# Kernel tuning notes

Measured on AMD Instinct MI355X. Metric: run time of the kernel, lower is better.

The kernel has to match this reference:

```python
import jax, jax.numpy as jnp
import numpy as np

EMBED_DIM = 1024
NUM_HEADS = 16
HEAD_DIM = EMBED_DIM // NUM_HEADS
MLP_HIDDEN = 4096


def layer_norm(x, gamma, beta, eps=1e-5):
    mu = jnp.mean(x, axis=-1, keepdims=True)
    var = jnp.var(x, axis=-1, keepdims=True)
    return (x - mu) / jnp.sqrt(var + eps) * gamma + beta


def setup_inputs() -> dict:
    key = jax.random.key(0)
    ks = jax.random.split(key, 16)
    d, h = EMBED_DIM, MLP_HIDDEN
    s = 0.02
    inp = {
        "x": jax.random.normal(ks[0], (2, 2048, d), dtype=jnp.float32),
        "ln1_g": jnp.ones((d,), jnp.float32),
        "ln1_b": jnp.zeros((d,), jnp.float32),
        "ln2_g": jnp.ones((d,), jnp.float32),
        "ln2_b": jnp.zeros((d,), jnp.float32),
        "Wq": jax.random.normal(ks[1], (d, d), jnp.float32) * s,
        "bq": jnp.zeros((d,), jnp.float32),
        "Wk": jax.random.normal(ks[2], (d, d), jnp.float32) * s,
        "bk": jnp.zeros((d,), jnp.float32),
        "Wv": jax.random.normal(ks[3], (d, d), jnp.float32) * s,
        "bv": jnp.zeros((d,), jnp.float32),
        "Wo": jax.random.normal(ks[4], (d, d), jnp.float32) * s,
        "bo": jnp.zeros((d,), jnp.float32),
        "W1": jax.random.normal(ks[5], (d, h), jnp.float32) * s,
        "b1": jnp.zeros((h,), jnp.float32),
        "W2": jax.random.normal(ks[6], (h, d), jnp.float32) * s,
        "b2": jnp.zeros((d,), jnp.float32),
    }
    return inp


def reference(x, ln1_g, ln1_b, ln2_g, ln2_b, Wq, bq, Wk, bk, Wv, bv, Wo, bo, W1, b1, W2, b2):
    B, T, C = x.shape
    H, Dh = NUM_HEADS, HEAD_DIM
    # attention branch
    xn = layer_norm(x, ln1_g, ln1_b)
    q = (xn @ Wq + bq).reshape(B, T, H, Dh).transpose(0, 2, 1, 3)  # [B,H,T,Dh]
    k = (xn @ Wk + bk).reshape(B, T, H, Dh).transpose(0, 2, 1, 3)
    v = (xn @ Wv + bv).reshape(B, T, H, Dh).transpose(0, 2, 1, 3)
    scores = jnp.einsum('bhtd,bhsd->bhts', q, k) / jnp.sqrt(jnp.float32(Dh))
    attn = jax.nn.softmax(scores, axis=-1)
    out = jnp.einsum('bhts,bhsd->bhtd', attn, v)
    out = out.transpose(0, 2, 1, 3).reshape(B, T, C)
    x = x + out @ Wo + bo
    # MLP branch
    xn2 = layer_norm(x, ln2_g, ln2_b)
    x = x + jax.nn.relu(xn2 @ W1 + b1) @ W2 + b2
    return x
```

## Files before the change

kernel.cpp:

```cpp
#include <hip/hip_runtime.h>

typedef float f32x4 __attribute__((ext_vector_type(4)));
typedef __bf16 bf16x8 __attribute__((ext_vector_type(8)));

constexpr int TT   = 2048;
constexpr int CC   = 1024;
constexpr int HIDN = 4096;
constexpr int MM   = 4096;
constexpr int NQKV = 3072;

union U84 { uint32_t u[4]; bf16x8 v; };

__device__ inline uint32_t cvt_pk_bf16(float lo, float hi) {
  uint32_t r;
  asm("v_cvt_pk_bf16_f32 %0, %1, %2" : "=v"(r) : "v"(lo), "v"(hi));
  return r;
}
__device__ inline ushort f2bf(float f) { return (ushort)(cvt_pk_bf16(f, 0.f) & 0xffffu); }
__device__ inline float bfbits2f(uint32_t bits) {
  union { uint32_t u; float f; } c; c.u = bits; return c.f;
}
__device__ inline float exp2_fast(float x) {
  float r;
  asm("v_exp_f32 %0, %1" : "=v"(r) : "v"(x));
  return r;
}

#define AS1C(p) ((__attribute__((address_space(1))) void*)(p))
#define AS3(p)  ((__attribute__((address_space(3))) void*)(p))

__global__ __launch_bounds__(256) void prep_weights(const float* __restrict__ Wq,
                                                    const float* __restrict__ Wk,
                                                    const float* __restrict__ Wv,
                                                    const float* __restrict__ Wo,
                                                    const float* __restrict__ W1,
                                                    const float* __restrict__ W2,
                                                    const float* __restrict__ bq,
                                                    const float* __restrict__ bk,
                                                    const float* __restrict__ bv,
                                                    const float* __restrict__ x,
                                                    const float* __restrict__ g1,
                                                    const float* __restrict__ b1v,
                                                    ushort* __restrict__ WqkvT,
                                                    ushort* __restrict__ WoT,
                                                    ushort* __restrict__ W1T,
                                                    ushort* __restrict__ W2T,
                                                    float* __restrict__ Bqkv,
                                                    ushort* __restrict__ Xn) {
  const int id = blockIdx.x;
  const int t = threadIdx.x;
  if (id >= 12300) {
    const int row = id - 12300;
    float4 v = reinterpret_cast<const float4*>(x + (size_t)row * CC)[t];
    float s  = v.x + v.y + v.z + v.w;
    float ss = v.x * v.x + v.y * v.y + v.z * v.z + v.w * v.w;
#pragma unroll
    for (int off = 32; off; off >>= 1) {
      s  += __shfl_down(s, off);
      ss += __shfl_down(ss, off);
    }
    __shared__ float red[16];
    const int wid = t >> 6, lane = t & 63;
    if (lane == 0) { red[wid] = s; red[8 + wid] = ss; }
    __syncthreads();
    if (t == 0) {
      red[0] = red[0] + red[1] + red[2] + red[3];
      red[8] = red[8] + red[9] + red[10] + red[11];
    }
    __syncthreads();
    const float mu   = red[0] * (1.0f / CC);
    const float var  = red[8] * (1.0f / CC) - mu * mu;
    const float rstd = rsqrtf(var + 1e-5f);
    float4 gg = reinterpret_cast<const float4*>(g1)[t];
    float4 bb = reinterpret_cast<const float4*>(b1v)[t];
    uint2 st;
    st.x = cvt_pk_bf16((v.x - mu) * rstd * gg.x + bb.x, (v.y - mu) * rstd * gg.y + bb.y);
    st.y = cvt_pk_bf16((v.z - mu) * rstd * gg.z + bb.z, (v.w - mu) * rstd * gg.w + bb.w);
    *reinterpret_cast<uint2*>(Xn + (size_t)row * CC + t * 4) = st;
    return;
  }
  if (id >= 12288) {
    const int i = (id - 12288) * 256 + t;
    Bqkv[i] = (i < 1024) ? bq[i] : ((i < 2048) ? bk[i - 1024] : bv[i - 2048]);
    return;
  }
  const float* W; ushort* out; int Kd, Nd, bx, by, rowOff = 0;
  if (id < 4096) {
    const int which = id >> 10, sub = id & 1023;
    bx = sub & 31; by = sub >> 5; Kd = 1024; Nd = 1024;
    if (which == 0)      { W = Wq; out = WqkvT; rowOff = 0; }
    else if (which == 1) { W = Wk; out = WqkvT; rowOff = 1024; }
    else if (which == 2) { W = Wv; out = WqkvT; rowOff = 2048; }
    else                 { W = Wo; out = WoT; }
  } else if (id < 8192) {
    const int sub = id - 4096; bx = sub & 127; by = sub >> 7;
    W = W1; out = W1T; Kd = 1024; Nd = 4096;
  } else {
    const int sub = id - 8192; bx = sub & 31; by = sub >> 5;
    W = W2; out = W2T; Kd = 4096; Nd = 1024;
  }
  const int n0 = bx * 32, k0 = by * 32;
  __shared__ float Ts[32][33];
  {
    const int r = t >> 3, cb = (t & 7) * 4;
    float4 v = *reinterpret_cast<const float4*>(W + (size_t)(k0 + r) * Nd + n0 + cb);
    Ts[r][cb + 0] = v.x; Ts[r][cb + 1] = v.y; Ts[r][cb + 2] = v.z; Ts[r][cb + 3] = v.w;
  }
  __syncthreads();
  {
    const int nl = t >> 3, kb = (t & 7) * 4;
    uint2 st;
    st.x = cvt_pk_bf16(Ts[kb + 0][nl], Ts[kb + 1][nl]);
    st.y = cvt_pk_bf16(Ts[kb + 2][nl], Ts[kb + 3][nl]);
    *reinterpret_cast<uint2*>(out + (size_t)(rowOff + n0 + nl) * Kd + k0 + kb) = st;
  }
}

template <int BN, bool RELU, bool VOUT, bool PARTIAL>
__global__ __launch_bounds__(512, 2) void gemm_8w(const ushort* __restrict__ A,
                                                  const ushort* __restrict__ Bt,
                                                  const float* __restrict__ bias,
                                                  ushort* __restrict__ outp,
                                                  ushort* __restrict__ Vt,
                                                  ushort* __restrict__ P1,
                                                  ushort* __restrict__ P2,
                                                  ushort* __restrict__ P3,
                                                  int N, int K, int Kchunk) {
  constexpr int WCOLS = BN / 4;
  constexpr int NF    = WCOLS / 16;
  constexpr int BCH   = BN / 64;
  constexpr int BUFB  = 32768 + BN * 128;
  __shared__ char lds[2 * BUFB];
  const int t = threadIdx.x, lane = t & 63, w = t >> 6;
  const int g = lane >> 4, i16 = lane & 15;
  const int wr = w >> 2, wc = w & 3;
  const int nwg  = gridDim.x * gridDim.y;
  const int orig = blockIdx.y * gridDim.x + blockIdx.x;
  const int sw   = (orig & 7) * (nwg >> 3) + (orig >> 3);
  const int row0 = (sw / gridDim.x) * 256, col0 = (sw % gridDim.x) * BN;
  const int kstart = PARTIAL ? blockIdx.z * Kchunk : 0;
  const int NT = (PARTIAL ? Kchunk : K) >> 6;
  ushort* __restrict__ Out = outp;
  if (PARTIAL) Out = (blockIdx.z == 0) ? outp : (blockIdx.z == 1) ? P1
              : (blockIdx.z == 2) ? P2 : P3;

  const ushort* aG[4];
  const ushort* bG[BCH];
#pragma unroll
  for (int i = 0; i < 4; ++i) {
    const int c = t + 512 * i;
    const int r = c >> 3, ssw = (c & 7) ^ (r & 7);
    aG[i] = A + (size_t)(row0 + r) * K + kstart + ssw * 8;
  }
#pragma unroll
  for (int i = 0; i < BCH; ++i) {
    const int c = t + 512 * i;
    const int r = c >> 3, ssw = (c & 7) ^ (r & 7);
    bG[i] = Bt + (size_t)(col0 + r) * K + kstart + ssw * 8;
  }

  int aoff[8][2], boff[NF][2];
#pragma unroll
  for (int mf = 0; mf < 8; ++mf) {
    const int R = wr * 128 + mf * 16 + i16;
#pragma unroll
    for (int kk = 0; kk < 2; ++kk)
      aoff[mf][kk] = R * 128 + (((kk << 2) | g) ^ (R & 7)) * 16;
  }
#pragma unroll
  for (int nf = 0; nf < NF; ++nf) {
    const int Cn = wc * WCOLS + nf * 16 + i16;
#pragma unroll
    for (int kk = 0; kk < 2; ++kk)
      boff[nf][kk] = Cn * 128 + (((kk << 2) | g) ^ (Cn & 7)) * 16;
  }

  f32x4 acc[8][NF] = {};

  auto STAGE = [&](int bi, int kt) {
    char* aB = lds + bi * BUFB;
    char* bB = aB + 32768;
    const int ko = kt * 64;
#pragma unroll
    for (int i = 0; i < 4; ++i)
      __builtin_amdgcn_global_load_lds(AS1C(aG[i] + ko), AS3(aB + i * 8192 + w * 1024), 16, 0, 0);
#pragma unroll
    for (int i = 0; i < BCH; ++i)
      __builtin_amdgcn_global_load_lds(AS1C(bG[i] + ko), AS3(bB + i * 8192 + w * 1024), 16, 0, 0);
  };

  STAGE(0, 0);

  for (int kt = 0; kt < NT; ++kt) {
    const int cur = kt & 1;
    if (kt + 1 < NT) {
      STAGE(cur ^ 1, kt + 1);
      if constexpr (BN == 256) asm volatile("s_waitcnt vmcnt(8)" ::: "memory");
      else                     asm volatile("s_waitcnt vmcnt(7)" ::: "memory");
    } else {
      asm volatile("s_waitcnt vmcnt(0)" ::: "memory");
    }
    asm volatile("s_barrier" ::: "memory");
    __builtin_amdgcn_sched_barrier(0);

    const char* aB = (const char*)lds + cur * BUFB;
    const char* bB = aB + 32768;
    bf16x8 b4[NF][2], a4[4][2];
#pragma unroll
    for (int nf = 0; nf < NF; ++nf)
#pragma unroll
      for (int kk = 0; kk < 2; ++kk)
        b4[nf][kk] = *reinterpret_cast<const bf16x8*>(bB + boff[nf][kk]);
#pragma unroll
    for (int mf = 0; mf < 4; ++mf)
#pragma unroll
      for (int kk = 0; kk < 2; ++kk)
        a4[mf][kk] = *reinterpret_cast<const bf16x8*>(aB + aoff[mf][kk]);
    __builtin_amdgcn_s_setprio(1);
#pragma unroll
    for (int mf = 0; mf < 4; ++mf)
#pragma unroll
      for (int nf = 0; nf < NF; ++nf)
#pragma unroll
        for (int kk = 0; kk < 2; ++kk)
          acc[mf][nf] = __builtin_amdgcn_mfma_f32_16x16x32_bf16(a4[mf][kk], b4[nf][kk], acc[mf][nf], 0, 0, 0);
    __builtin_amdgcn_s_setprio(0);
    asm volatile("s_barrier" ::: "memory");
    __builtin_amdgcn_sched_barrier(0);
#pragma unroll
    for (int mf = 0; mf < 4; ++mf)
#pragma unroll
      for (int kk = 0; kk < 2; ++kk)
        a4[mf][kk] = *reinterpret_cast<const bf16x8*>(aB + aoff[mf + 4][kk]);
    __builtin_amdgcn_s_setprio(1);
#pragma unroll
    for (int mf = 0; mf < 4; ++mf)
#pragma unroll
      for (int nf = 0; nf < NF; ++nf)
#pragma unroll
        for (int kk = 0; kk < 2; ++kk)
          acc[mf + 4][nf] = __builtin_amdgcn_mfma_f32_16x16x32_bf16(a4[mf][kk], b4[nf][kk], acc[mf + 4][nf], 0, 0, 0);
    __builtin_amdgcn_s_setprio(0);
    asm volatile("s_barrier" ::: "memory");
    __builtin_amdgcn_sched_barrier(0);
  }

  const int qcol0 = col0 + wc * WCOLS;

  if constexpr (VOUT) {
#pragma unroll
    for (int nf = 0; nf < NF; ++nf) {
      const int ncol = qcol0 + nf * 16 + i16;
      const float bb = bias[ncol];
      if (ncol >= 2048) {
        const int d = ncol - 2048;
        const int hh = d >> 6, dd = d & 63;
#pragma unroll
        for (int mf = 0; mf < 8; ++mf) {
          const int mrow = row0 + wr * 128 + mf * 16 + 4 * g;
          const int bb_ = mrow >> 11, tok = mrow & 2047;
          uint2 st;
          st.x = cvt_pk_bf16(acc[mf][nf][0] + bb, acc[mf][nf][1] + bb);
          st.y = cvt_pk_bf16(acc[mf][nf][2] + bb, acc[mf][nf][3] + bb);
          *reinterpret_cast<uint2*>(Vt + (size_t)((bb_ * 16 + hh) * 64 + dd) * TT + tok) = st;
        }
      } else {
#pragma unroll
        for (int mf = 0; mf < 8; ++mf) {
          const int mrow = row0 + wr * 128 + mf * 16 + 4 * g;
#pragma unroll
          for (int r = 0; r < 4; ++r)
            Out[(size_t)(mrow + r) * N + ncol] = f2bf(acc[mf][nf][r] + bb);
        }
      }
    }
    return;
  } else {
    float* Lf = (float*)(lds + w * 4096);
    const int rr2 = lane >> 2, q = lane & 3;
#pragma unroll
    for (int mf = 0; mf < 8; ++mf) {
#pragma unroll
      for (int nf = 0; nf < NF; ++nf)
#pragma unroll
        for (int r = 0; r < 4; ++r) {
          const int row = 4 * g + r;
          Lf[row * 64 + ((16 * nf + i16) ^ ((row & 7) << 2))] = acc[mf][nf][r];
        }
      asm volatile("s_waitcnt lgkmcnt(0)" ::: "memory");
      uint32_t u[8];
#pragma unroll
      for (int j = 0; j < 4; ++j) {
        f32x4 v = *reinterpret_cast<const f32x4*>(Lf + rr2 * 64 + ((q * 16 + 4 * j) ^ ((rr2 & 7) << 2)));
        float e0 = v[0], e1 = v[1], e2 = v[2], e3 = v[3];
        if (!PARTIAL) {
          const float4 b4v = *reinterpret_cast<const float4*>(bias + qcol0 + q * 16 + 4 * j);
          e0 += b4v.x; e1 += b4v.y; e2 += b4v.z; e3 += b4v.w;
          if (RELU) {
            e0 = fmaxf(e0, 0.f); e1 = fmaxf(e1, 0.f);
            e2 = fmaxf(e2, 0.f); e3 = fmaxf(e3, 0.f);
          }
        }
        u[2 * j + 0] = cvt_pk_bf16(e0, e1);
        u[2 * j + 1] = cvt_pk_bf16(e2, e3);
      }
      const int mrow = row0 + wr * 128 + mf * 16 + rr2;
      ushort* orow = Out + (size_t)mrow * N + qcol0 + q * 16;
      uint4 s0; s0.x = u[0]; s0.y = u[1]; s0.z = u[2]; s0.w = u[3];
      uint4 s1; s1.x = u[4]; s1.y = u[5]; s1.z = u[6]; s1.w = u[7];
      *reinterpret_cast<uint4*>(orow) = s0;
      *reinterpret_cast<uint4*>(orow + 8) = s1;
      asm volatile("s_waitcnt lgkmcnt(0)" ::: "memory");
    }
  }
}

__device__ inline float bfsum4(uint32_t a, uint32_t b, uint32_t c, uint32_t d, bool hi) {
  if (hi) return bfbits2f(a & 0xffff0000u) + bfbits2f(b & 0xffff0000u) +
                 bfbits2f(c & 0xffff0000u) + bfbits2f(d & 0xffff0000u);
  return bfbits2f(a << 16) + bfbits2f(b << 16) + bfbits2f(c << 16) + bfbits2f(d << 16);
}

__global__ __launch_bounds__(256) void reduce_wo_ln(const ushort* __restrict__ P0,
                                                    const ushort* __restrict__ P1,
                                                    const ushort* __restrict__ P2,
                                                    const ushort* __restrict__ P3,
                                                    const float* __restrict__ x,
                                                    const float* __restrict__ bo,
                                                    const float* __restrict__ g,
                                                    const float* __restrict__ b,
                                                    float* __restrict__ X1f,
                                                    ushort* __restrict__ Xn) {
  const int row = blockIdx.x, t = threadIdx.x;
  const size_t off = (size_t)row * CC + t * 4;
  float4 v  = *reinterpret_cast<const float4*>(x + off);
  const uint2 q0 = *reinterpret_cast<const uint2*>(P0 + off);
  const uint2 q1 = *reinterpret_cast<const uint2*>(P1 + off);
  const uint2 q2 = *reinterpret_cast<const uint2*>(P2 + off);
  const uint2 q3 = *reinterpret_cast<const uint2*>(P3 + off);
  float4 bb = reinterpret_cast<const float4*>(bo)[t];
  v.x += bfsum4(q0.x, q1.x, q2.x, q3.x, false) + bb.x;
  v.y += bfsum4(q0.x, q1.x, q2.x, q3.x, true)  + bb.y;
  v.z += bfsum4(q0.y, q1.y, q2.y, q3.y, false) + bb.z;
  v.w += bfsum4(q0.y, q1.y, q2.y, q3.y, true)  + bb.w;
  *reinterpret_cast<float4*>(X1f + off) = v;

  float s  = v.x + v.y + v.z + v.w;
  float ss = v.x * v.x + v.y * v.y + v.z * v.z + v.w * v.w;
#pragma unroll
  for (int o = 32; o; o >>= 1) {
    s  += __shfl_down(s, o);
    ss += __shfl_down(ss, o);
  }
  __shared__ float red[16];
  const int wid = t >> 6, lane = t & 63;
  if (lane == 0) { red[wid] = s; red[8 + wid] = ss; }
  __syncthreads();
  if (t == 0) {
    red[0] = red[0] + red[1] + red[2] + red[3];
    red[8] = red[8] + red[9] + red[10] + red[11];
  }
  __syncthreads();
  const float mu   = red[0] * (1.0f / CC);
  const float var  = red[8] * (1.0f / CC) - mu * mu;
  const float rstd = rsqrtf(var + 1e-5f);
  float4 gg = reinterpret_cast<const float4*>(g)[t];
  float4 lb = reinterpret_cast<const float4*>(b)[t];
  uint2 st;
  st.x = cvt_pk_bf16((v.x - mu) * rstd * gg.x + lb.x, (v.y - mu) * rstd * gg.y + lb.y);
  st.y = cvt_pk_bf16((v.z - mu) * rstd * gg.z + lb.z, (v.w - mu) * rstd * gg.w + lb.w);
  *reinterpret_cast<uint2*>(Xn + off) = st;
}

__global__ __launch_bounds__(256) void reduce_fc2(const ushort* __restrict__ P0,
                                                  const ushort* __restrict__ P1,
                                                  const ushort* __restrict__ P2,
                                                  const ushort* __restrict__ P3,
                                                  const float* __restrict__ X1,
                                                  const float* __restrict__ b2,
                                                  float* __restrict__ out) {
  const int row = blockIdx.x, t = threadIdx.x;
  const size_t off = (size_t)row * CC + t * 4;
  float4 v  = *reinterpret_cast<const float4*>(X1 + off);
  const uint2 q0 = *reinterpret_cast<const uint2*>(P0 + off);
  const uint2 q1 = *reinterpret_cast<const uint2*>(P1 + off);
  const uint2 q2 = *reinterpret_cast<const uint2*>(P2 + off);
  const uint2 q3 = *reinterpret_cast<const uint2*>(P3 + off);
  float4 bb = reinterpret_cast<const float4*>(b2)[t];
  v.x += bfsum4(q0.x, q1.x, q2.x, q3.x, false) + bb.x;
  v.y += bfsum4(q0.x, q1.x, q2.x, q3.x, true)  + bb.y;
  v.z += bfsum4(q0.y, q1.y, q2.y, q3.y, false) + bb.z;
  v.w += bfsum4(q0.y, q1.y, q2.y, q3.y, true)  + bb.w;
  *reinterpret_cast<float4*>(out + off) = v;
}

__global__ __launch_bounds__(512, 4) void attn_full(const ushort* __restrict__ qkv,
                                                    const ushort* __restrict__ Vt,
                                                    ushort* __restrict__ attnb) {
  __shared__ ushort Ks[2][4096];
  __shared__ ushort Vs[2][4096];
  __shared__ uint32_t Ps[8][16][36];
  const int t = threadIdx.x, lane = t & 63, w = t >> 6;
  const int g = lane >> 4, iq = lane & 15;
  const int flat = blockIdx.x;
  const int work = (flat & 7) * 64 + (flat >> 3);
  const int bh = work >> 4;
  const int qt = work & 15;
  const int b = bh >> 4, h = bh & 15;

  bf16x8 qfrag[2];
  {
    const ushort* qrow = qkv + (size_t)(b * TT + qt * 128 + w * 16 + iq) * NQKV + h * 64;
    const float qs = 0.125f * 1.44269504f;
#pragma unroll
    for (int kk = 0; kk < 2; ++kk) {
      uint4 raw = *reinterpret_cast<const uint4*>(qrow + kk * 32 + g * 8);
      uint32_t rr[4] = {raw.x, raw.y, raw.z, raw.w};
      U84 tmp;
#pragma unroll
      for (int c = 0; c < 4; ++c) {
        float lo = bfbits2f(rr[c] << 16) * qs;
        float hi = bfbits2f(rr[c] & 0xffff0000u) * qs;
        tmp.u[c] = cvt_pk_bf16(lo, hi);
      }
      qfrag[kk] = tmp.v;
    }
  }

  const int sr1 = t >> 3, sc1 = t & 7;
  const int csw = (sc1 ^ (sr1 & 7)) * 8;
  const ushort* kbase = qkv + 1024 + h * 64;
  const ushort* vbase = Vt + (size_t)(bh * 64) * TT;

  auto STAGE = [&](int bi, int kt) {
    const size_t tok = (size_t)(b * TT + kt * 64);
    __builtin_amdgcn_global_load_lds(AS1C(kbase + (tok + sr1) * NQKV + csw),
                                     AS3((char*)&Ks[bi][0] + w * 1024), 16, 0, 0);
    __builtin_amdgcn_global_load_lds(AS1C(vbase + (size_t)sr1 * TT + kt * 64 + csw),
                                     AS3((char*)&Vs[bi][0] + w * 1024), 16, 0, 0);
  };

  uint32_t (*pw)[36] = Ps[w];
  const int wsw = (iq & 8) << 1;
  const int xsb = wsw << 2;
  const char* prow = (const char*)&pw[iq][0];

  float lrun = 0.f;
  f32x4 ot[4] = {};

  constexpr int NKT = TT / 64;
  STAGE(0, 0);

  for (int kt = 0; kt < NKT; ++kt) {
    const int cur = kt & 1;
    if (kt + 1 < NKT) {
      STAGE(cur ^ 1, kt + 1);
      asm volatile("s_waitcnt vmcnt(2)" ::: "memory");
    } else {
      asm volatile("s_waitcnt vmcnt(0)" ::: "memory");
    }
    asm volatile("s_barrier" ::: "memory");
    __builtin_amdgcn_sched_barrier(0);
    const char* Kc = (const char*)&Ks[cur][0];
    const char* Vc = (const char*)&Vs[cur][0];

    f32x4 sfr[4] = {};
    __builtin_amdgcn_s_setprio(1);
#pragma unroll
    for (int kk = 0; kk < 2; ++kk)
#pragma unroll
      for (int jf = 0; jf < 4; ++jf) {
        const int row = iq + 16 * jf;
        const int off = row * 128 + ((kk * 64 + g * 16) ^ ((row & 7) << 4));
        bf16x8 a = *reinterpret_cast<const bf16x8*>(Kc + off);
        sfr[jf] = __builtin_amdgcn_mfma_f32_16x16x32_bf16(a, qfrag[kk], sfr[jf], 0, 0, 0);
      }
    __builtin_amdgcn_s_setprio(0);

#pragma unroll
    for (int f = 0; f < 4; ++f) {
      float p0 = exp2_fast(sfr[f][0]);
      float p1 = exp2_fast(sfr[f][1]);
      float p2 = exp2_fast(sfr[f][2]);
      float p3 = exp2_fast(sfr[f][3]);
      lrun += (p0 + p1) + (p2 + p3);
      uint2 st2;
      st2.x = cvt_pk_bf16(p0, p1);
      st2.y = cvt_pk_bf16(p2, p3);
      *reinterpret_cast<uint2*>(&pw[iq][(8 * f + 2 * g) ^ wsw]) = st2;
    }
    asm volatile("s_waitcnt lgkmcnt(0)" ::: "memory");

    __builtin_amdgcn_s_setprio(1);
#pragma unroll
    for (int kk = 0; kk < 2; ++kk) {
      bf16x8 pb = *reinterpret_cast<const bf16x8*>(prow + ((kk * 64 + g * 16) ^ xsb));
#pragma unroll
      for (int df = 0; df < 4; ++df) {
        const int row = iq + 16 * df;
        const int off = row * 128 + ((kk * 64 + g * 16) ^ ((row & 7) << 4));
        bf16x8 a = *reinterpret_cast<const bf16x8*>(Vc + off);
        ot[df] = __builtin_amdgcn_mfma_f32_16x16x32_bf16(a, pb, ot[df], 0, 0, 0);
      }
    }
    __builtin_amdgcn_s_setprio(0);

    asm volatile("s_barrier" ::: "memory");
    __builtin_amdgcn_sched_barrier(0);
  }

  lrun += __shfl_xor(lrun, 16, 64);
  lrun += __shfl_xor(lrun, 32, 64);
  const int grow = b * TT + qt * 128 + w * 16 + iq;
  const float inv = 1.f / lrun;
  ushort* orow = attnb + (size_t)grow * CC + h * 64;
#pragma unroll
  for (int df = 0; df < 4; ++df) {
    uint2 st;
    st.x = cvt_pk_bf16(ot[df][0] * inv, ot[df][1] * inv);
    st.y = cvt_pk_bf16(ot[df][2] * inv, ot[df][3] * inv);
    *reinterpret_cast<uint2*>(orow + df * 16 + g * 4) = st;
  }
}

extern "C" void kernel_launch(void* const* d_in, const int* in_sizes, int n_in,
                              void* d_out, int out_size, void* d_ws, size_t ws_size,
                              hipStream_t stream) {
  const float* x     = (const float*)d_in[0];
  const float* ln1_g = (const float*)d_in[1];
  const float* ln1_b = (const float*)d_in[2];
  const float* ln2_g = (const float*)d_in[3];
  const float* ln2_b = (const float*)d_in[4];
  const float* Wq = (const float*)d_in[5];
  const float* bq = (const float*)d_in[6];
  const float* Wk = (const float*)d_in[7];
  const float* bk = (const float*)d_in[8];
  const float* Wv = (const float*)d_in[9];
  const float* bv = (const float*)d_in[10];
  const float* Wo = (const float*)d_in[11];
  const float* bo = (const float*)d_in[12];
  const float* W1 = (const float*)d_in[13];
  const float* b1 = (const float*)d_in[14];
  const float* W2 = (const float*)d_in[15];
  const float* b2 = (const float*)d_in[16];
  float* out = (float*)d_out;
  char* ws = (char*)d_ws;

  ushort* WqkvT = (ushort*)(ws + 0);
  ushort* WoT   = (ushort*)(ws + 6291456);
  ushort* W1T   = (ushort*)(ws + 8388608);
  ushort* W2T   = (ushort*)(ws + 16777216);
  float*  Bqkv  = (float*) (ws + 25165824);
  ushort* Xn    = (ushort*)(ws + 25178112);
  ushort* Attn  = (ushort*)(ws + 33566720);
  float*  X1f   = (float*) (ws + 41955328);
  ushort* Qkv   = (ushort*)(ws + 58732544);
  ushort* Vtb   = (ushort*)(ws + 83898368);
  ushort* Hid   = (ushort*)(ws + 58732544);
  ushort* WoP0  = (ushort*)(ws + 58732544);
  ushort* WoP1  = (ushort*)(ws + 67121152);
  ushort* WoP2  = (ushort*)(ws + 75509760);
  ushort* WoP3  = (ushort*)(ws + 83898368);
  ushort* F2P0  = (ushort*)(ws + 0);
  ushort* F2P1  = (ushort*)(ws + 8388608);
  ushort* F2P2  = (ushort*)(ws + 25178112);
  ushort* F2P3  = (ushort*)(ws + 33566720);

  const dim3 blk(256);

  prep_weights<<<dim3(16396), blk, 0, stream>>>(Wq, Wk, Wv, Wo, W1, W2, bq, bk, bv,
                                                x, ln1_g, ln1_b,
                                                WqkvT, WoT, W1T, W2T, Bqkv, Xn);
  gemm_8w<192, false, true, false><<<dim3(16, 16), dim3(512), 0, stream>>>(
      Xn, WqkvT, Bqkv, Qkv, Vtb, nullptr, nullptr, nullptr, NQKV, 1024, 0);
  attn_full<<<dim3(512), dim3(512), 0, stream>>>(Qkv, Vtb, Attn);
  gemm_8w<256, false, false, true><<<dim3(4, 16, 4), dim3(512), 0, stream>>>(
      Attn, WoT, nullptr, WoP0, nullptr, WoP1, WoP2, WoP3, 1024, 1024, 256);
  reduce_wo_ln<<<dim3(MM), blk, 0, stream>>>(WoP0, WoP1, WoP2, WoP3, x, bo, ln2_g, ln2_b, X1f, Xn);
  gemm_8w<256, true, false, false><<<dim3(16, 16), dim3(512), 0, stream>>>(
      Xn, W1T, b1, Hid, nullptr, nullptr, nullptr, nullptr, HIDN, 1024, 0);
  gemm_8w<256, false, false, true><<<dim3(4, 16, 4), dim3(512), 0, stream>>>(
      Hid, W2T, nullptr, F2P0, nullptr, F2P1, F2P2, F2P3, 1024, 4096, 1024);
  reduce_fc2<<<dim3(MM), blk, 0, stream>>>(F2P0, F2P1, F2P2, F2P3, X1f, b2, out);
}
```

Baseline: 222.6 us.

## Use BN=128 tiles with 2-way split-K for Wo and FC2 GEMMs

```diff
diff --git a/kernel.cpp b/kernel.cpp
--- a/kernel.cpp
+++ b/kernel.cpp
@@ -123,8 +123,6 @@
                                                   ushort* __restrict__ outp,
                                                   ushort* __restrict__ Vt,
                                                   ushort* __restrict__ P1,
-                                                  ushort* __restrict__ P2,
-                                                  ushort* __restrict__ P3,
                                                   int N, int K, int Kchunk) {
   constexpr int WCOLS = BN / 4;
   constexpr int NF    = WCOLS / 16;
@@ -140,9 +138,7 @@
   const int row0 = (sw / gridDim.x) * 256, col0 = (sw % gridDim.x) * BN;
   const int kstart = PARTIAL ? blockIdx.z * Kchunk : 0;
   const int NT = (PARTIAL ? Kchunk : K) >> 6;
-  ushort* __restrict__ Out = outp;
-  if (PARTIAL) Out = (blockIdx.z == 0) ? outp : (blockIdx.z == 1) ? P1
-              : (blockIdx.z == 2) ? P2 : P3;
+  ushort* __restrict__ Out = (PARTIAL && blockIdx.z) ? P1 : outp;
 
   const ushort* aG[4];
   const ushort* bG[BCH];
@@ -195,8 +191,9 @@
     const int cur = kt & 1;
     if (kt + 1 < NT) {
       STAGE(cur ^ 1, kt + 1);
-      if constexpr (BN == 256) asm volatile("s_waitcnt vmcnt(8)" ::: "memory");
-      else                     asm volatile("s_waitcnt vmcnt(7)" ::: "memory");
+      if constexpr (BN == 256)      asm volatile("s_waitcnt vmcnt(8)" ::: "memory");
+      else if constexpr (BN == 192) asm volatile("s_waitcnt vmcnt(7)" ::: "memory");
+      else                          asm volatile("s_waitcnt vmcnt(6)" ::: "memory");
     } else {
       asm volatile("s_waitcnt vmcnt(0)" ::: "memory");
     }
@@ -272,6 +269,19 @@
           for (int r = 0; r < 4; ++r)
             Out[(size_t)(mrow + r) * N + ncol] = f2bf(acc[mf][nf][r] + bb);
         }
+      }
+    }
+    return;
+  } else if constexpr (BN == 128) {
+#pragma unroll
+    for (int nf = 0; nf < NF; ++nf) {
+      const int ncol = qcol0 + nf * 16 + i16;
+#pragma unroll
+      for (int mf = 0; mf < 8; ++mf) {
+        const int mrow = row0 + wr * 128 + mf * 16 + 4 * g;
+#pragma unroll
+        for (int r = 0; r < 4; ++r)
+          Out[(size_t)(mrow + r) * N + ncol] = f2bf(acc[mf][nf][r]);
       }
     }
     return;
@@ -315,16 +325,13 @@
   }
 }
 
-__device__ inline float bfsum4(uint32_t a, uint32_t b, uint32_t c, uint32_t d, bool hi) {
-  if (hi) return bfbits2f(a & 0xffff0000u) + bfbits2f(b & 0xffff0000u) +
-                 bfbits2f(c & 0xffff0000u) + bfbits2f(d & 0xffff0000u);
-  return bfbits2f(a << 16) + bfbits2f(b << 16) + bfbits2f(c << 16) + bfbits2f(d << 16);
+__device__ inline float bfsum2(uint32_t a, uint32_t b, bool hi) {
+  if (hi) return bfbits2f(a & 0xffff0000u) + bfbits2f(b & 0xffff0000u);
+  return bfbits2f(a << 16) + bfbits2f(b << 16);
 }
 
 __global__ __launch_bounds__(256) void reduce_wo_ln(const ushort* __restrict__ P0,
                                                     const ushort* __restrict__ P1,
-                                                    const ushort* __restrict__ P2,
-                                                    const ushort* __restrict__ P3,
                                                     const float* __restrict__ x,
                                                     const float* __restrict__ bo,
                                                     const float* __restrict__ g,
@@ -336,13 +343,11 @@
   float4 v  = *reinterpret_cast<const float4*>(x + off);
   const uint2 q0 = *reinterpret_cast<const uint2*>(P0 + off);
   const uint2 q1 = *reinterpret_cast<const uint2*>(P1 + off);
-  const uint2 q2 = *reinterpret_cast<const uint2*>(P2 + off);
-  const uint2 q3 = *reinterpret_cast<const uint2*>(P3 + off);
   float4 bb = reinterpret_cast<const float4*>(bo)[t];
-  v.x += bfsum4(q0.x, q1.x, q2.x, q3.x, false) + bb.x;
-  v.y += bfsum4(q0.x, q1.x, q2.x, q3.x, true)  + bb.y;
-  v.z += bfsum4(q0.y, q1.y, q2.y, q3.y, false) + bb.z;
-  v.w += bfsum4(q0.y, q1.y, q2.y, q3.y, true)  + bb.w;
+  v.x += bfsum2(q0.x, q1.x, false) + bb.x;
+  v.y += bfsum2(q0.x, q1.x, true)  + bb.y;
+  v.z += bfsum2(q0.y, q1.y, false) + bb.z;
+  v.w += bfsum2(q0.y, q1.y, true)  + bb.w;
   *reinterpret_cast<float4*>(X1f + off) = v;
 
   float s  = v.x + v.y + v.z + v.w;
@@ -374,8 +379,6 @@
 
 __global__ __launch_bounds__(256) void reduce_fc2(const ushort* __restrict__ P0,
                                                   const ushort* __restrict__ P1,
-                                                  const ushort* __restrict__ P2,
-                                                  const ushort* __restrict__ P3,
                                                   const float* __restrict__ X1,
                                                   const float* __restrict__ b2,
                                                   float* __restrict__ out) {
@@ -384,13 +387,11 @@
   float4 v  = *reinterpret_cast<const float4*>(X1 + off);
   const uint2 q0 = *reinterpret_cast<const uint2*>(P0 + off);
   const uint2 q1 = *reinterpret_cast<const uint2*>(P1 + off);
-  const uint2 q2 = *reinterpret_cast<const uint2*>(P2 + off);
-  const uint2 q3 = *reinterpret_cast<const uint2*>(P3 + off);
   float4 bb = reinterpret_cast<const float4*>(b2)[t];
-  v.x += bfsum4(q0.x, q1.x, q2.x, q3.x, false) + bb.x;
-  v.y += bfsum4(q0.x, q1.x, q2.x, q3.x, true)  + bb.y;
-  v.z += bfsum4(q0.y, q1.y, q2.y, q3.y, false) + bb.z;
-  v.w += bfsum4(q0.y, q1.y, q2.y, q3.y, true)  + bb.w;
+  v.x += bfsum2(q0.x, q1.x, false) + bb.x;
+  v.y += bfsum2(q0.x, q1.x, true)  + bb.y;
+  v.z += bfsum2(q0.y, q1.y, false) + bb.z;
+  v.w += bfsum2(q0.y, q1.y, true)  + bb.w;
   *reinterpret_cast<float4*>(out + off) = v;
 }
 
@@ -559,12 +560,8 @@
   ushort* Hid   = (ushort*)(ws + 58732544);
   ushort* WoP0  = (ushort*)(ws + 58732544);
   ushort* WoP1  = (ushort*)(ws + 67121152);
-  ushort* WoP2  = (ushort*)(ws + 75509760);
-  ushort* WoP3  = (ushort*)(ws + 83898368);
   ushort* F2P0  = (ushort*)(ws + 0);
   ushort* F2P1  = (ushort*)(ws + 8388608);
-  ushort* F2P2  = (ushort*)(ws + 25178112);
-  ushort* F2P3  = (ushort*)(ws + 33566720);
 
   const dim3 blk(256);
 
@@ -572,14 +569,14 @@
                                                 x, ln1_g, ln1_b,
                                                 WqkvT, WoT, W1T, W2T, Bqkv, Xn);
   gemm_8w<192, false, true, false><<<dim3(16, 16), dim3(512), 0, stream>>>(
-      Xn, WqkvT, Bqkv, Qkv, Vtb, nullptr, nullptr, nullptr, NQKV, 1024, 0);
+      Xn, WqkvT, Bqkv, Qkv, Vtb, nullptr, NQKV, 1024, 0);
   attn_full<<<dim3(512), dim3(512), 0, stream>>>(Qkv, Vtb, Attn);
-  gemm_8w<256, false, false, true><<<dim3(4, 16, 4), dim3(512), 0, stream>>>(
-      Attn, WoT, nullptr, WoP0, nullptr, WoP1, WoP2, WoP3, 1024, 1024, 256);
-  reduce_wo_ln<<<dim3(MM), blk, 0, stream>>>(WoP0, WoP1, WoP2, WoP3, x, bo, ln2_g, ln2_b, X1f, Xn);
+  gemm_8w<128, false, false, true><<<dim3(8, 16, 2), dim3(512), 0, stream>>>(
+      Attn, WoT, nullptr, WoP0, nullptr, WoP1, 1024, 1024, 512);
+  reduce_wo_ln<<<dim3(MM), blk, 0, stream>>>(WoP0, WoP1, x, bo, ln2_g, ln2_b, X1f, Xn);
   gemm_8w<256, true, false, false><<<dim3(16, 16), dim3(512), 0, stream>>>(
-      Xn, W1T, b1, Hid, nullptr, nullptr, nullptr, nullptr, HIDN, 1024, 0);
-  gemm_8w<256, false, false, true><<<dim3(4, 16, 4), dim3(512), 0, stream>>>(
-      Hid, W2T, nullptr, F2P0, nullptr, F2P1, F2P2, F2P3, 1024, 4096, 1024);
-  reduce_fc2<<<dim3(MM), blk, 0, stream>>>(F2P0, F2P1, F2P2, F2P3, X1f, b2, out);
-}
+      Xn, W1T, b1, Hid, nullptr, nullptr, HIDN, 1024, 0);
+  gemm_8w<128, false, false, true><<<dim3(8, 16, 2), dim3(512), 0, stream>>>(
+      Hid, W2T, nullptr, F2P0, nullptr, F2P1, 1024, 4096, 2048);
+  reduce_fc2<<<dim3(MM), blk, 0, stream>>>(F2P0, F2P1, X1f, b2, out);
+}
```

Measured after the change: 215.8 us. 1.03x faster.
